# Performance work log

Hardware: AMD Instinct MI355X
Metric: run time of the kernel (lower is better)

## Reference

```python
import jax, jax.numpy as jnp
import numpy as np

EPS = 1e-5  # torch BatchNorm1d default eps

N_NODES = 100000
N_EDGES = 1250000
N_GRAPHS = 512
F_IN = 16
HID = 64


def _bn(x, w, b):
    # track_running_stats=False, momentum=None -> always batch statistics (biased var)
    m = jnp.mean(x, axis=0)
    v = jnp.var(x, axis=0)
    return (x - m) * jax.lax.rsqrt(v + EPS) * w + b


def _prelu(x, a):
    return jnp.where(x >= 0, x, a * x)


def _gcn_conv(x, W, b, src, dst, n):
    # PyG GCNConv: h = x W; add self loops; sym-norm by deg^-1/2 on target degrees
    h = x @ W  # [N, out]
    ones = jnp.ones(src.shape[0], x.dtype)
    deg = jax.ops.segment_sum(ones, dst, num_segments=n) + 1.0  # +1 self loop
    dis = jax.lax.rsqrt(deg)  # deg >= 1 so finite
    norm = (dis[src] * dis[dst])[:, None]  # [E,1]
    agg = jax.ops.segment_sum(h[src] * norm, dst, num_segments=n)
    # self-loop contribution: norm = dis[i]*dis[i]
    return agg + h * (dis * dis)[:, None] + b


def setup_inputs() -> dict:
    key = jax.random.key(0)
    ks = jax.random.split(key, 12)
    x = jax.random.normal(ks[0], (N_NODES, F_IN), dtype=jnp.float32)
    edge_index = jax.random.randint(ks[1], (2, N_EDGES), 0, N_NODES, dtype=jnp.int32)
    # evenly spaced graph ids so every segment is non-empty (global_max_pool)
    batch = ((jnp.arange(N_NODES, dtype=jnp.int32) * N_GRAPHS) // N_NODES).astype(jnp.int32)
    s = 0.1
    W1 = jax.random.normal(ks[2], (F_IN, HID), jnp.float32) * s
    b1 = jnp.zeros((HID,), jnp.float32)
    W2 = jax.random.normal(ks[3], (HID, HID), jnp.float32) * s
    b2 = jnp.zeros((HID,), jnp.float32)
    lw1 = jax.random.normal(ks[4], (HID, HID), jnp.float32) * s
    lb1 = jnp.zeros((HID,), jnp.float32)
    lw2 = jax.random.normal(ks[5], (HID, 1), jnp.float32) * s
    lb2 = jnp.zeros((1,), jnp.float32)
    bn1_w = jnp.ones((HID,), jnp.float32); bn1_b = jnp.zeros((HID,), jnp.float32)
    bn2_w = jnp.ones((HID,), jnp.float32); bn2_b = jnp.zeros((HID,), jnp.float32)
    bn3_w = jnp.ones((HID,), jnp.float32); bn3_b = jnp.zeros((HID,), jnp.float32)
    bn4_w = jnp.ones((1,), jnp.float32); bn4_b = jnp.zeros((1,), jnp.float32)
    a1 = jnp.full((1,), 0.25, jnp.float32)
    a2 = jnp.full((1,), 0.25, jnp.float32)
    a3 = jnp.full((1,), 0.25, jnp.float32)
    a4 = jnp.full((1,), 0.25, jnp.float32)
    return {"x": x, "edge_index": edge_index, "batch": batch,
            "W1": W1, "b1": b1, "W2": W2, "b2": b2,
            "bn1_w": bn1_w, "bn1_b": bn1_b, "bn2_w": bn2_w, "bn2_b": bn2_b,
            "bn3_w": bn3_w, "bn3_b": bn3_b, "bn4_w": bn4_w, "bn4_b": bn4_b,
            "lw1": lw1, "lb1": lb1, "lw2": lw2, "lb2": lb2,
            "a1": a1, "a2": a2, "a3": a3, "a4": a4}


def reference(x, edge_index, batch, W1, b1, W2, b2,
              bn1_w, bn1_b, bn2_w, bn2_b, bn3_w, bn3_b, bn4_w, bn4_b,
              lw1, lb1, lw2, lb2, a1, a2, a3, a4):
    src, dst = edge_index[0], edge_index[1]
    n = x.shape[0]
    h = _gcn_conv(x, W1, b1, src, dst, n)
    h = _prelu(_bn(h, bn1_w, bn1_b), a1)
    h = _gcn_conv(h, W2, b2, src, dst, n)
    h = _prelu(_bn(h, bn2_w, bn2_b), a2)
    g = jax.ops.segment_max(h, batch, num_segments=N_GRAPHS)  # global_max_pool
    g = _prelu(_bn(g @ lw1 + lb1, bn3_w, bn3_b), a3)
    g = _prelu(_bn(g @ lw2 + lb2, bn4_w, bn4_b), a4)
    return g
```

## Files before the change

### kernel.cpp

```cpp
#include <hip/hip_runtime.h>
#include <hip/hip_bf16.h>

#define N_NODES 100000
#define N_EDGES 1250000
#define N_GRAPHS 512
#define F_IN 16
#define HID 64
#define EPS 1e-5f

#define K_B 1563
#define B_H 250
#define EPB 5000
#define M_SC (K_B * B_H)

typedef unsigned int uint;

__device__ __forceinline__ uint f2bf(float f) {
    uint u = __float_as_uint(f);
    return (u + 0x7fffu + ((u >> 16) & 1u)) >> 16;
}
__device__ __forceinline__ uint pack2(float lo, float hi) {
    return f2bf(lo) | (f2bf(hi) << 16);
}
__device__ __forceinline__ void unpack8(float* o, uint4 v) {
    o[0] = __uint_as_float(v.x << 16); o[1] = __uint_as_float(v.x & 0xffff0000u);
    o[2] = __uint_as_float(v.y << 16); o[3] = __uint_as_float(v.y & 0xffff0000u);
    o[4] = __uint_as_float(v.z << 16); o[5] = __uint_as_float(v.z & 0xffff0000u);
    o[6] = __uint_as_float(v.w << 16); o[7] = __uint_as_float(v.w & 0xffff0000u);
}
__device__ __forceinline__ void accum8(float* a, uint4 v) {
    a[0] += __uint_as_float(v.x << 16); a[1] += __uint_as_float(v.x & 0xffff0000u);
    a[2] += __uint_as_float(v.y << 16); a[3] += __uint_as_float(v.y & 0xffff0000u);
    a[4] += __uint_as_float(v.z << 16); a[5] += __uint_as_float(v.z & 0xffff0000u);
    a[6] += __uint_as_float(v.w << 16); a[7] += __uint_as_float(v.w & 0xffff0000u);
}


__global__ __launch_bounds__(256) void k_hist(const int4* __restrict__ dst4,
                                              int* __restrict__ hist) {
    __shared__ int h[K_B];
    int t = threadIdx.x, b = blockIdx.x;
    for (int k = t; k < K_B; k += 256) h[k] = 0;
    __syncthreads();
    const int4* d4 = dst4 + b * (EPB / 4);
    for (int i = t; i < EPB / 4; i += 256) {
        int4 d = d4[i];
        atomicAdd(&h[d.x >> 6], 1);
        atomicAdd(&h[d.y >> 6], 1);
        atomicAdd(&h[d.z >> 6], 1);
        atomicAdd(&h[d.w >> 6], 1);
    }
    __syncthreads();
    for (int k = t; k < K_B; k += 256) hist[k * B_H + b] = h[k];
}

__global__ void k_s1(const int* __restrict__ in, int* __restrict__ out,
                     int* __restrict__ bsum, int n) {
    __shared__ int sh[256];
    int blk = blockIdx.x, t = threadIdx.x;
    int base = blk * 1024 + t * 4;
    int v[4];
#pragma unroll
    for (int j = 0; j < 4; j++) { int i = base + j; v[j] = (i < n) ? in[i] : 0; }
    int tsum = v[0] + v[1] + v[2] + v[3];
    sh[t] = tsum;
    __syncthreads();
    for (int ofs = 1; ofs < 256; ofs <<= 1) {
        int x = (t >= ofs) ? sh[t - ofs] : 0;
        __syncthreads();
        sh[t] += x;
        __syncthreads();
    }
    int run = sh[t] - tsum;
    if (t == 255) bsum[blk] = sh[255];
#pragma unroll
    for (int j = 0; j < 4; j++) { int i = base + j; if (i < n) out[i] = run; run += v[j]; }
}

__global__ void k_s2(int* __restrict__ bsum, int nb) {
    __shared__ int sh[512];
    int t = threadIdx.x;
    int v = (t < nb) ? bsum[t] : 0;
    sh[t] = v;
    __syncthreads();
    for (int ofs = 1; ofs < 512; ofs <<= 1) {
        int x = (t >= ofs) ? sh[t - ofs] : 0;
        __syncthreads();
        sh[t] += x;
        __syncthreads();
    }
    if (t < nb) bsum[t] = sh[t] - v;
}

__global__ __launch_bounds__(256) void k_bucketize(const int4* __restrict__ src4,
        const int4* __restrict__ dst4, const int* __restrict__ ebase,
        const int* __restrict__ bsum, int* __restrict__ ebuck) {
    __shared__ int base[K_B];
    int t = threadIdx.x, b = blockIdx.x;
    for (int k = t; k < K_B; k += 256) {
        int idx = k * B_H + b;
        base[k] = ebase[idx] + bsum[idx >> 10];
    }
    __syncthreads();
    const int4* s4 = src4 + b * (EPB / 4);
    const int4* d4 = dst4 + b * (EPB / 4);
    for (int i = t; i < EPB / 4; i += 256) {
        int4 s = s4[i];
        int4 d = d4[i];
        int p;
        p = atomicAdd(&base[d.x >> 6], 1); ebuck[p] = s.x | ((d.x & 63) << 17);
        p = atomicAdd(&base[d.y >> 6], 1); ebuck[p] = s.y | ((d.y & 63) << 17);
        p = atomicAdd(&base[d.z >> 6], 1); ebuck[p] = s.z | ((d.z & 63) << 17);
        p = atomicAdd(&base[d.w >> 6], 1); ebuck[p] = s.w | ((d.w & 63) << 17);
    }
}

__global__ __launch_bounds__(256) void k_csr(const int* __restrict__ ebase,
        const int* __restrict__ bsum, const int* __restrict__ ebuck,
        int* __restrict__ col, int2* __restrict__ meta, float* __restrict__ dis) {
    int k = blockIdx.x, t = threadIdx.x;
    int i0 = k * B_H;
    int beg = ebase[i0] + bsum[i0 >> 10];
    int end;
    if (k + 1 < K_B) {
        int i1 = (k + 1) * B_H;
        end = ebase[i1] + bsum[i1 >> 10];
    } else {
        end = N_EDGES;
    }
    int m = end - beg;
    __shared__ int c[64];
    __shared__ int sb[64];
    if (t < 64) c[t] = 0;
    __syncthreads();
    for (int i = t; i < m; i += 256) atomicAdd(&c[ebuck[beg + i] >> 17], 1);
    __syncthreads();
    if (t < 64) {
        int v = c[t];
        int incl = v;
#pragma unroll
        for (int o = 1; o < 64; o <<= 1) { int u = __shfl_up(incl, o); if (t >= o) incl += u; }
        int excl = incl - v;
        int node = k * 64 + t;
        if (node < N_NODES) {
            meta[node] = make_int2(beg + excl, v);
            dis[node] = rsqrtf((float)v + 1.0f);
        }
        sb[t] = beg + excl;
    }
    __syncthreads();
    for (int i = t; i < m; i += 256) {
        int e = ebuck[beg + i];
        int pos = atomicAdd(&sb[e >> 17], 1);
        col[pos] = e & 0x1FFFF;
    }
}


__global__ __launch_bounds__(512) void k_gemm1(const float* __restrict__ x,
        const float* __restrict__ W1, const float* __restrict__ dis,
        ushort* __restrict__ A) {
    __shared__ float Ws[F_IN * HID];
    __shared__ float xs[32 * F_IN];
    int t = threadIdx.x;
    Ws[t] = W1[t];
    Ws[t + 512] = W1[t + 512];
    int n0 = blockIdx.x * 32;
    xs[t] = x[n0 * F_IN + t];
    __syncthreads();
    int f = t & 63, w = t >> 6;
    float Wreg[F_IN];
#pragma unroll
    for (int k = 0; k < F_IN; k++) Wreg[k] = Ws[k * HID + f];
#pragma unroll
    for (int i = 0; i < 4; i++) {
        int nl = w * 4 + i;
        float acc = 0.f;
#pragma unroll
        for (int kq = 0; kq < 4; kq++) {
            const float4 xv = *(const float4*)&xs[nl * F_IN + kq * 4];
            acc = fmaf(xv.x, Wreg[4 * kq + 0], acc);
            acc = fmaf(xv.y, Wreg[4 * kq + 1], acc);
            acc = fmaf(xv.z, Wreg[4 * kq + 2], acc);
            acc = fmaf(xv.w, Wreg[4 * kq + 3], acc);
        }
        int n = n0 + nl;
        A[(size_t)n * HID + f] = (ushort)f2bf(acc * dis[n]);
    }
}

__global__ __launch_bounds__(512) void k_gemm2(const ushort* __restrict__ B,
        const float* __restrict__ s1r, const float* __restrict__ ss1r,
        const float* __restrict__ bnw, const float* __restrict__ bnb,
        const float* __restrict__ alpha, const float* __restrict__ W2,
        const float* __restrict__ dis, ushort* __restrict__ A2) {
    __shared__ float Ws[HID * HID];
    __shared__ float xs[32 * HID];
    __shared__ float scs[64], shsv[64];
    int t = threadIdx.x;
#pragma unroll
    for (int i = 0; i < 8; i++) Ws[i * 512 + t] = W2[i * 512 + t];
    if (t < 64) {
        float s = 0, q = 0;
#pragma unroll
        for (int r = 0; r < 8; r++) { s += s1r[r * 64 + t]; q += ss1r[r * 64 + t]; }
        const float invn = 1.f / N_NODES;
        float m = s * invn;
        float v = q * invn - m * m;
        float sc = bnw[t] * rsqrtf(v + EPS);
        scs[t] = sc;
        shsv[t] = bnb[t] - m * sc;
    }
    __syncthreads();
    int n0 = blockIdx.x * 32;
    float al = alpha[0];
    {
        const uint* Bu = (const uint*)(B + (size_t)n0 * HID);
#pragma unroll
        for (int i = 0; i < 2; i++) {
            int idx = i * 512 + t;
            uint u = Bu[idx];
            int fp = (idx & 31) * 2;
            int row = idx >> 5;
            float lo = __uint_as_float(u << 16) * scs[fp] + shsv[fp];
            float hi = __uint_as_float(u & 0xffff0000u) * scs[fp + 1] + shsv[fp + 1];
            lo = lo >= 0.f ? lo : al * lo;
            hi = hi >= 0.f ? hi : al * hi;
            xs[row * HID + fp] = lo;
            xs[row * HID + fp + 1] = hi;
        }
    }
    __syncthreads();
    int f = t & 63, w = t >> 6;
    float Wreg[HID];
#pragma unroll
    for (int k = 0; k < HID; k++) Wreg[k] = Ws[k * HID + f];
#pragma unroll
    for (int i = 0; i < 4; i++) {
        int nl = w * 4 + i;
        float acc = 0.f;
#pragma unroll
        for (int kq = 0; kq < 16; kq++) {
            const float4 xv = *(const float4*)&xs[nl * HID + kq * 4];
            acc = fmaf(xv.x, Wreg[4 * kq + 0], acc);
            acc = fmaf(xv.y, Wreg[4 * kq + 1], acc);
            acc = fmaf(xv.z, Wreg[4 * kq + 2], acc);
            acc = fmaf(xv.w, Wreg[4 * kq + 3], acc);
        }
        int n = n0 + nl;
        A2[(size_t)n * HID + f] = (ushort)f2bf(acc * dis[n]);
    }
}

__global__ __launch_bounds__(256) void k_agg(const uint4* __restrict__ Asc,
        const float* __restrict__ dis, const int2* __restrict__ meta,
        const int* __restrict__ col, const float* __restrict__ bias,
        uint4* __restrict__ outB, float* __restrict__ sumr,
        float* __restrict__ sumsqr) {
    int t = threadIdx.x;
    int nid = blockIdx.x * 32 + (t >> 3);
    int fq = t & 7;
    int2 mt = meta[nid];
    int beg = mt.x, m = mt.y;
    float acc[8] = {0, 0, 0, 0, 0, 0, 0, 0};
    int j = 0;
    for (; j + 4 <= m; j += 4) {
        int s0 = col[beg + j];
        int s1 = col[beg + j + 1];
        int s2 = col[beg + j + 2];
        int s3 = col[beg + j + 3];
        uint4 r0 = Asc[(size_t)s0 * 8 + fq];
        uint4 r1 = Asc[(size_t)s1 * 8 + fq];
        uint4 r2 = Asc[(size_t)s2 * 8 + fq];
        uint4 r3 = Asc[(size_t)s3 * 8 + fq];
        accum8(acc, r0);
        accum8(acc, r1);
        accum8(acc, r2);
        accum8(acc, r3);
    }
    for (; j < m; ++j) {
        int s = col[beg + j];
        accum8(acc, Asc[(size_t)s * 8 + fq]);
    }
    accum8(acc, Asc[(size_t)nid * 8 + fq]);
    float dn = dis[nid];
    float4 b0 = ((const float4*)bias)[fq * 2];
    float4 b1 = ((const float4*)bias)[fq * 2 + 1];
    float o[8];
    o[0] = b0.x + dn * acc[0]; o[1] = b0.y + dn * acc[1];
    o[2] = b0.z + dn * acc[2]; o[3] = b0.w + dn * acc[3];
    o[4] = b1.x + dn * acc[4]; o[5] = b1.y + dn * acc[5];
    o[6] = b1.z + dn * acc[6]; o[7] = b1.w + dn * acc[7];
    uint4 ov;
    ov.x = pack2(o[0], o[1]); ov.y = pack2(o[2], o[3]);
    ov.z = pack2(o[4], o[5]); ov.w = pack2(o[6], o[7]);
    outB[(size_t)nid * 8 + fq] = ov;

    float sq[8];
#pragma unroll
    for (int i = 0; i < 8; i++) sq[i] = o[i] * o[i];
#pragma unroll
    for (int ofs = 8; ofs <= 32; ofs <<= 1) {
#pragma unroll
        for (int i = 0; i < 8; i++) {
            o[i] += __shfl_xor(o[i], ofs);
            sq[i] += __shfl_xor(sq[i], ofs);
        }
    }
    __shared__ float ps[4][64], pq[4][64];
    int w = t >> 6, lane = t & 63;
    if (lane < 8) {
#pragma unroll
        for (int i = 0; i < 8; i++) {
            ps[w][lane * 8 + i] = o[i];
            pq[w][lane * 8 + i] = sq[i];
        }
    }
    __syncthreads();
    if (t < 64) {
        float a = ps[0][t] + ps[1][t] + ps[2][t] + ps[3][t];
        float b = pq[0][t] + pq[1][t] + pq[2][t] + pq[3][t];
        int rep = (blockIdx.x & 7) * 64;
        atomicAdd(&sumr[rep + t], a);
        atomicAdd(&sumsqr[rep + t], b);
    }
}

__global__ __launch_bounds__(256) void k_pool(const uint4* __restrict__ a,
        const float* __restrict__ s2r, const float* __restrict__ ss2r,
        const float* __restrict__ bnw, const float* __restrict__ bnb,
        const float* __restrict__ alpha, const float* __restrict__ lw1,
        const float* __restrict__ lb1, float* __restrict__ th,
        float* __restrict__ s3r, float* __restrict__ ss3r) {
    __shared__ float scs[64], shsv[64];
    __shared__ float sm[2048];
    __shared__ float gr[64];
    int gi = blockIdx.x;
    int t = threadIdx.x, rg = t >> 3, fq = t & 7;
    if (t < 64) {
        float s = 0, q = 0;
#pragma unroll
        for (int r = 0; r < 8; r++) { s += s2r[r * 64 + t]; q += ss2r[r * 64 + t]; }
        const float invn = 1.f / N_NODES;
        float m = s * invn;
        float v = q * invn - m * m;
        float sc = bnw[t] * rsqrtf(v + EPS);
        scs[t] = sc;
        shsv[t] = bnb[t] - m * sc;
    }
    __syncthreads();
    int lo = (gi * N_NODES + N_GRAPHS - 1) / N_GRAPHS;
    int hi = ((gi + 1) * N_NODES + N_GRAPHS - 1) / N_GRAPHS;
    float al = alpha[0];
    float sc[8], sh[8];
#pragma unroll
    for (int i = 0; i < 8; i++) { sc[i] = scs[fq * 8 + i]; sh[i] = shsv[fq * 8 + i]; }
    float mx[8];
#pragma unroll
    for (int i = 0; i < 8; i++) mx[i] = -INFINITY;
    for (int r = lo + rg; r < hi; r += 32) {
        float o[8];
        unpack8(o, a[(size_t)r * 8 + fq]);
#pragma unroll
        for (int i = 0; i < 8; i++) {
            float v = o[i] * sc[i] + sh[i];
            v = v >= 0.f ? v : al * v;
            mx[i] = fmaxf(mx[i], v);
        }
    }
#pragma unroll
    for (int i = 0; i < 8; i++) sm[rg * 64 + fq * 8 + i] = mx[i];
    __syncthreads();
    if (t < 64) {
        float m = sm[t];
#pragma unroll
        for (int i = 1; i < 32; i++) m = fmaxf(m, sm[i * 64 + t]);
        gr[t] = m;
    }
    __syncthreads();
    if (t < 64) {
        float acc = lb1[t];
#pragma unroll
        for (int k = 0; k < 64; k++) acc = fmaf(gr[k], lw1[k * 64 + t], acc);
        th[gi * 64 + t] = acc;
        int rep = (gi & 7) * 64;
        atomicAdd(&s3r[rep + t], acc);
        atomicAdd(&ss3r[rep + t], acc * acc);
    }
}

__global__ __launch_bounds__(512) void k_head(const float* __restrict__ th,
        const float* __restrict__ s3r, const float* __restrict__ ss3r,
        const float* __restrict__ bn3w, const float* __restrict__ bn3b,
        const float* __restrict__ a3, const float* __restrict__ lw2,
        const float* __restrict__ lb2, const float* __restrict__ bn4w,
        const float* __restrict__ bn4b, const float* __restrict__ a4,
        float* __restrict__ out) {
    int t = threadIdx.x, w = t >> 6, lane = t & 63;
    __shared__ float t2s[N_GRAPHS];
    __shared__ float rs[8], rq[8];
    const float invn = 1.f / N_GRAPHS;
    float s = 0, q = 0;
#pragma unroll
    for (int r = 0; r < 8; r++) { s += s3r[r * 64 + lane]; q += ss3r[r * 64 + lane]; }
    float m3 = s * invn;
    float v3 = q * invn - m3 * m3;
    float sc3 = bn3w[lane] * rsqrtf(v3 + EPS);
    float sh3 = bn3b[lane] - m3 * sc3;
    float al3 = a3[0];
    float wv = lw2[lane];
    float lb = lb2[0];
    for (int r = w; r < N_GRAPHS; r += 8) {
        float xv = th[r * 64 + lane] * sc3 + sh3;
        xv = xv >= 0.f ? xv : al3 * xv;
        float p = xv * wv;
#pragma unroll
        for (int o = 32; o > 0; o >>= 1) p += __shfl_xor(p, o);
        if (lane == 0) t2s[r] = p + lb;
    }
    __syncthreads();
    float tv = t2s[t];
    float ps = tv, pq = tv * tv;
#pragma unroll
    for (int o = 32; o > 0; o >>= 1) { ps += __shfl_xor(ps, o); pq += __shfl_xor(pq, o); }
    if (lane == 0) { rs[w] = ps; rq[w] = pq; }
    __syncthreads();
    float S = 0, Q = 0;
#pragma unroll
    for (int i = 0; i < 8; i++) { S += rs[i]; Q += rq[i]; }
    float m4 = S * invn;
    float v4 = Q * invn - m4 * m4;
    float sc4 = bn4w[0] * rsqrtf(v4 + EPS);
    float xb = (tv - m4) * sc4 + bn4b[0];
    float al4 = a4[0];
    out[t] = xb >= 0.f ? xb : al4 * xb;
}

extern "C" void kernel_launch(void* const* d_in, const int* in_sizes, int n_in,
                              void* d_out, int out_size, void* d_ws, size_t ws_size,
                              hipStream_t stream) {
    const float* x   = (const float*)d_in[0];
    const int*   ei  = (const int*)d_in[1];
    const int4*  src4 = (const int4*)ei;
    const int4*  dst4 = (const int4*)(ei + N_EDGES);
    const float* W1  = (const float*)d_in[3];
    const float* b1  = (const float*)d_in[4];
    const float* W2  = (const float*)d_in[5];
    const float* b2  = (const float*)d_in[6];
    const float* bn1w = (const float*)d_in[7];
    const float* bn1b = (const float*)d_in[8];
    const float* bn2w = (const float*)d_in[9];
    const float* bn2b = (const float*)d_in[10];
    const float* bn3w = (const float*)d_in[11];
    const float* bn3b = (const float*)d_in[12];
    const float* bn4w = (const float*)d_in[13];
    const float* bn4b = (const float*)d_in[14];
    const float* lw1  = (const float*)d_in[15];
    const float* lb1  = (const float*)d_in[16];
    const float* lw2  = (const float*)d_in[17];
    const float* lb2  = (const float*)d_in[18];
    const float* a1   = (const float*)d_in[19];
    const float* a2   = (const float*)d_in[20];
    const float* a3   = (const float*)d_in[21];
    const float* a4   = (const float*)d_in[22];
    float* out = (float*)d_out;

    char* p = (char*)d_ws;
    auto carve = [&](size_t bytes) -> void* {
        void* r = (void*)p;
        p += (bytes + 255) & ~(size_t)255;
        return r;
    };
    int*    hist = (int*)carve((size_t)M_SC * 4);
    int*    ebase = (int*)carve((size_t)M_SC * 4);
    int*    ebuck = (int*)carve((size_t)N_EDGES * 4);
    int*    col  = (int*)carve((size_t)N_EDGES * 4);
    float*  dis  = (float*)carve((size_t)N_NODES * 4);
    int2*   meta = (int2*)carve((size_t)N_NODES * 8);
    int*    bsum = (int*)carve(2048);
    ushort* A    = (ushort*)carve((size_t)N_NODES * HID * 2);
    ushort* B    = (ushort*)carve((size_t)N_NODES * HID * 2);
    float*  th   = (float*)carve((size_t)N_GRAPHS * HID * 4);
    float*  statsr = (float*)carve(6 * 512 * 4);
    float* s1r = statsr,          *ss1r = statsr + 512;
    float* s2r = statsr + 1024,   *ss2r = statsr + 1536;
    float* s3r = statsr + 2048,   *ss3r = statsr + 2560;

    hipMemsetAsync(statsr, 0, 6 * 512 * 4, stream);

    const int SC_BLKS = (M_SC + 1023) / 1024;

    k_hist<<<B_H, 256, 0, stream>>>(dst4, hist);
    k_s1<<<SC_BLKS, 256, 0, stream>>>(hist, ebase, bsum, M_SC);
    k_s2<<<1, 512, 0, stream>>>(bsum, SC_BLKS);
    k_bucketize<<<B_H, 256, 0, stream>>>(src4, dst4, ebase, bsum, ebuck);
    k_csr<<<K_B, 256, 0, stream>>>(ebase, bsum, ebuck, col, meta, dis);

    const int NB32 = N_NODES / 32;
    k_gemm1<<<NB32, 512, 0, stream>>>(x, W1, dis, A);
    k_agg<<<NB32, 256, 0, stream>>>((const uint4*)A, dis, meta, col, b1, (uint4*)B,
                                    s1r, ss1r);
    k_gemm2<<<NB32, 512, 0, stream>>>(B, s1r, ss1r, bn1w, bn1b, a1, W2, dis, A);
    k_agg<<<NB32, 256, 0, stream>>>((const uint4*)A, dis, meta, col, b2, (uint4*)B,
                                    s2r, ss2r);
    k_pool<<<N_GRAPHS, 256, 0, stream>>>((const uint4*)B, s2r, ss2r, bn2w, bn2b, a2,
                                         lw1, lb1, th, s3r, ss3r);
    k_head<<<1, 512, 0, stream>>>(th, s3r, ss3r, bn3w, bn3b, a3, lw2, lb2,
                                  bn4w, bn4b, a4, out);
}
```

Before: 181.5 us.

## Double histogram blocks, fold memset into hist, cache buckets in LDS, unroll aggregation

```diff
diff --git a/kernel.cpp b/kernel.cpp
--- a/kernel.cpp
+++ b/kernel.cpp
@@ -9,8 +9,8 @@
 #define EPS 1e-5f
 
 #define K_B 1563
-#define B_H 250
-#define EPB 5000
+#define B_H 500
+#define EPB 2500
 #define M_SC (K_B * B_H)
 
 typedef unsigned int uint;
@@ -37,9 +37,13 @@
 
 
 __global__ __launch_bounds__(256) void k_hist(const int4* __restrict__ dst4,
-                                              int* __restrict__ hist) {
+                                              int* __restrict__ hist,
+                                              float* __restrict__ statsr) {
     __shared__ int h[K_B];
     int t = threadIdx.x, b = blockIdx.x;
+    if (b == 0) {
+        for (int i = t; i < 6 * 512; i += 256) statsr[i] = 0.f;
+    }
     for (int k = t; k < K_B; k += 256) h[k] = 0;
     __syncthreads();
     const int4* d4 = dst4 + b * (EPB / 4);
@@ -78,18 +82,22 @@
 }
 
 __global__ void k_s2(int* __restrict__ bsum, int nb) {
-    __shared__ int sh[512];
+    __shared__ int sh[256];
     int t = threadIdx.x;
-    int v = (t < nb) ? bsum[t] : 0;
-    sh[t] = v;
-    __syncthreads();
-    for (int ofs = 1; ofs < 512; ofs <<= 1) {
+    int v[4]; int s = 0;
+#pragma unroll
+    for (int j = 0; j < 4; j++) { int i = t * 4 + j; v[j] = (i < nb) ? bsum[i] : 0; s += v[j]; }
+    sh[t] = s;
+    __syncthreads();
+    for (int ofs = 1; ofs < 256; ofs <<= 1) {
         int x = (t >= ofs) ? sh[t - ofs] : 0;
         __syncthreads();
         sh[t] += x;
         __syncthreads();
     }
-    if (t < nb) bsum[t] = sh[t] - v;
+    int run = sh[t] - s;
+#pragma unroll
+    for (int j = 0; j < 4; j++) { int i = t * 4 + j; if (i < nb) bsum[i] = run; run += v[j]; }
 }
 
 __global__ __launch_bounds__(256) void k_bucketize(const int4* __restrict__ src4,
@@ -123,17 +131,26 @@
     int beg = ebase[i0] + bsum[i0 >> 10];
     int end;
     if (k + 1 < K_B) {
-        int i1 = (k + 1) * B_H;
+        int i1 = i0 + B_H;
         end = ebase[i1] + bsum[i1 >> 10];
     } else {
         end = N_EDGES;
     }
     int m = end - beg;
+    __shared__ int eb[2048];
     __shared__ int c[64];
     __shared__ int sb[64];
     if (t < 64) c[t] = 0;
     __syncthreads();
-    for (int i = t; i < m; i += 256) atomicAdd(&c[ebuck[beg + i] >> 17], 1);
+    if (m <= 2048) {
+        for (int i = t; i < m; i += 256) {
+            int e = ebuck[beg + i];
+            eb[i] = e;
+            atomicAdd(&c[e >> 17], 1);
+        }
+    } else {
+        for (int i = t; i < m; i += 256) atomicAdd(&c[ebuck[beg + i] >> 17], 1);
+    }
     __syncthreads();
     if (t < 64) {
         int v = c[t];
@@ -149,10 +166,18 @@
         sb[t] = beg + excl;
     }
     __syncthreads();
-    for (int i = t; i < m; i += 256) {
-        int e = ebuck[beg + i];
-        int pos = atomicAdd(&sb[e >> 17], 1);
-        col[pos] = e & 0x1FFFF;
+    if (m <= 2048) {
+        for (int i = t; i < m; i += 256) {
+            int e = eb[i];
+            int pos = atomicAdd(&sb[e >> 17], 1);
+            col[pos] = e & 0x1FFFF;
+        }
+    } else {
+        for (int i = t; i < m; i += 256) {
+            int e = ebuck[beg + i];
+            int pos = atomicAdd(&sb[e >> 17], 1);
+            col[pos] = e & 0x1FFFF;
+        }
     }
 }
 
@@ -264,21 +289,34 @@
     int beg = mt.x, m = mt.y;
     float acc[8] = {0, 0, 0, 0, 0, 0, 0, 0};
     int j = 0;
-    for (; j + 4 <= m; j += 4) {
+    for (; j + 8 <= m; j += 8) {
         int s0 = col[beg + j];
         int s1 = col[beg + j + 1];
         int s2 = col[beg + j + 2];
         int s3 = col[beg + j + 3];
+        int s4 = col[beg + j + 4];
+        int s5 = col[beg + j + 5];
+        int s6 = col[beg + j + 6];
+        int s7 = col[beg + j + 7];
         uint4 r0 = Asc[(size_t)s0 * 8 + fq];
         uint4 r1 = Asc[(size_t)s1 * 8 + fq];
         uint4 r2 = Asc[(size_t)s2 * 8 + fq];
         uint4 r3 = Asc[(size_t)s3 * 8 + fq];
-        accum8(acc, r0);
-        accum8(acc, r1);
-        accum8(acc, r2);
-        accum8(acc, r3);
-    }
-    for (; j < m; ++j) {
+        uint4 r4 = Asc[(size_t)s4 * 8 + fq];
+        uint4 r5 = Asc[(size_t)s5 * 8 + fq];
+        uint4 r6 = Asc[(size_t)s6 * 8 + fq];
+        uint4 r7 = Asc[(size_t)s7 * 8 + fq];
+        accum8(acc, r0); accum8(acc, r1); accum8(acc, r2); accum8(acc, r3);
+        accum8(acc, r4); accum8(acc, r5); accum8(acc, r6); accum8(acc, r7);
+    }
+    for (; j + 2 <= m; j += 2) {
+        int s0 = col[beg + j];
+        int s1 = col[beg + j + 1];
+        uint4 r0 = Asc[(size_t)s0 * 8 + fq];
+        uint4 r1 = Asc[(size_t)s1 * 8 + fq];
+        accum8(acc, r0); accum8(acc, r1);
+    }
+    if (j < m) {
         int s = col[beg + j];
         accum8(acc, Asc[(size_t)s * 8 + fq]);
     }
@@ -477,7 +515,7 @@
     int*    col  = (int*)carve((size_t)N_EDGES * 4);
     float*  dis  = (float*)carve((size_t)N_NODES * 4);
     int2*   meta = (int2*)carve((size_t)N_NODES * 8);
-    int*    bsum = (int*)carve(2048);
+    int*    bsum = (int*)carve(4096);
     ushort* A    = (ushort*)carve((size_t)N_NODES * HID * 2);
     ushort* B    = (ushort*)carve((size_t)N_NODES * HID * 2);
     float*  th   = (float*)carve((size_t)N_GRAPHS * HID * 4);
@@ -486,13 +524,11 @@
     float* s2r = statsr + 1024,   *ss2r = statsr + 1536;
     float* s3r = statsr + 2048,   *ss3r = statsr + 2560;
 
-    hipMemsetAsync(statsr, 0, 6 * 512 * 4, stream);
-
     const int SC_BLKS = (M_SC + 1023) / 1024;
 
-    k_hist<<<B_H, 256, 0, stream>>>(dst4, hist);
+    k_hist<<<B_H, 256, 0, stream>>>(dst4, hist, statsr);
     k_s1<<<SC_BLKS, 256, 0, stream>>>(hist, ebase, bsum, M_SC);
-    k_s2<<<1, 512, 0, stream>>>(bsum, SC_BLKS);
+    k_s2<<<1, 256, 0, stream>>>(bsum, SC_BLKS);
     k_bucketize<<<B_H, 256, 0, stream>>>(src4, dst4, ebase, bsum, ebuck);
     k_csr<<<K_B, 256, 0, stream>>>(ebase, bsum, ebuck, col, meta, dis);
 
```

Result: no change. 183.9 us (+1.3%).
